# Kernel tuning notes

Hardware: AMD Instinct MI355X
Metric: run time of the kernel (lower is better)

Reference implementation:

```python
import jax, jax.numpy as jnp
import numpy as np

V, E, H = 50000, 200, 256
B, R, S, W = 16, 16, 16, 32


def gru_last(x, Wih, Whh, bih, bhh):
    """PyTorch-style GRU, return final hidden state.
    x: [N, T, D]; Wih: [3H, D]; Whh: [3H, H]. Gate order: r, z, n."""
    gx = jnp.einsum('ntd,gd->ntg', x, Wih) + bih  # precompute input gates [N,T,3H]
    h0 = jnp.zeros((x.shape[0], Whh.shape[1]), x.dtype)

    def step(h, gxt):
        gh = h @ Whh.T + bhh
        xr, xz, xn = jnp.split(gxt, 3, axis=-1)
        hr, hz, hn = jnp.split(gh, 3, axis=-1)
        r = jax.nn.sigmoid(xr + hr)
        z = jax.nn.sigmoid(xz + hz)
        n = jnp.tanh(xn + r * hn)
        return (1.0 - z) * n + z * h, None

    h, _ = jax.lax.scan(step, h0, jnp.swapaxes(gx, 0, 1))
    return h  # [N, H]


def mlp(x, W1, b1, W2, b2):
    # Linear -> SELU -> (Dropout is identity in eval) -> Linear
    return jax.nn.selu(x @ W1.T + b1) @ W2.T + b2


def setup_inputs() -> dict:
    key = jax.random.key(0)
    ks = jax.random.split(key, 20)
    n = lambda k, shp: (jax.random.normal(k, shp, dtype=jnp.float32) * 0.05)
    inp = {
        'inputs': jax.random.randint(ks[0], (B, R, S, W), 0, V, dtype=jnp.int64),
        'emb': n(ks[1], (V, E)),
        'w_Wih': n(ks[2], (3 * H, E)), 'w_Whh': n(ks[3], (3 * H, H)),
        'w_bih': n(ks[4], (3 * H,)), 'w_bhh': n(ks[5], (3 * H,)),
        's_Wih': n(ks[6], (3 * H, H)), 's_Whh': n(ks[7], (3 * H, H)),
        's_bih': n(ks[8], (3 * H,)), 's_bhh': n(ks[9], (3 * H,)),
        'r_Wih': n(ks[10], (3 * H, H)), 'r_Whh': n(ks[11], (3 * H, H)),
        'r_bih': n(ks[12], (3 * H,)), 'r_bhh': n(ks[13], (3 * H,)),
        'rfc_W1': n(ks[14], (H // 2, H)), 'rfc_b1': n(ks[15], (H // 2,)),
        'rfc_W2': n(ks[16], (1, H // 2)), 'rfc_b2': jnp.zeros((1,), jnp.float32),
        'pfc_W1': n(ks[17], (H // 2, H)), 'pfc_b1': n(ks[18], (H // 2,)),
        'pfc_W2': n(ks[19], (1, H // 2)), 'pfc_b2': jnp.zeros((1,), jnp.float32),
    }
    return inp


def reference(inputs, emb, w_Wih, w_Whh, w_bih, w_bhh,
              s_Wih, s_Whh, s_bih, s_bhh,
              r_Wih, r_Whh, r_bih, r_bhh,
              rfc_W1, rfc_b1, rfc_W2, rfc_b2,
              pfc_W1, pfc_b1, pfc_W2, pfc_b2):
    b, r, s, w = inputs.shape
    x = emb[inputs]                                   # [B,R,S,W,E] (dropout = identity in eval)
    # word-level GRU over all sentences at once (batches the Python double loop)
    sent_h = gru_last(x.reshape(b * r * s, w, E), w_Wih, w_Whh, w_bih, w_bhh)  # [B*R*S, H]
    # sentence-level GRU per review
    rev_h = gru_last(sent_h.reshape(b * r, s, H), s_Wih, s_Whh, s_bih, s_bhh)  # [B*R, H]
    p_batch = rev_h.reshape(b, r, H)                  # [B, R, H]
    r_stars = mlp(p_batch, rfc_W1, rfc_b1, rfc_W2, rfc_b2)  # [B, R, 1]
    # review-level GRU per business
    biz_h = gru_last(p_batch, r_Wih, r_Whh, r_bih, r_bhh)   # [B, H]
    b_stars = mlp(biz_h, pfc_W1, pfc_b1, pfc_W2, pfc_b2)    # [B, 1]
    return (b_stars, r_stars)
```

## Files before the change

### kernel.cpp

```cpp
#include <hip/hip_runtime.h>
#include <math.h>

#define VOCAB 50000
#define EDIM  200
#define HDIM  256
#define G3    768
#define NSEQ1 4096
#define T1    32
#define NSEQ2 256
#define T2    16
#define NSEQ3 16
#define T3    16

using bf16x8 = __attribute__((ext_vector_type(8))) short;
using f32x4  = __attribute__((ext_vector_type(4))) float;

__device__ __forceinline__ float sigmoid_f(float x) {
    return 1.0f / (1.0f + __expf(-x));
}
__device__ __forceinline__ float tanh_f(float x) {
    return 1.0f - 2.0f / (__expf(2.0f * x) + 1.0f);
}
__device__ __forceinline__ short f2b(float f) {
    unsigned u = __float_as_uint(f);
    unsigned r = (u + 0x7fffu + ((u >> 16) & 1u)) >> 16;
    return (short)r;
}
__device__ __forceinline__ float b2f(unsigned short v) {
    return __uint_as_float((unsigned)v << 16);
}
__device__ __forceinline__ void lds_barrier() {
    asm volatile("s_waitcnt lgkmcnt(0)\n\ts_barrier" ::: "memory");
}

struct CvtJob { const float* src; short* dst; int kin; int kpad; };
struct CvtJobs { CvtJob j[6]; };

__global__ void convert6(CvtJobs jobs) {
    const CvtJob jb = jobs.j[blockIdx.y];
    const int r = blockIdx.x;
    for (int k = threadIdx.x; k < jb.kpad; k += blockDim.x)
        jb.dst[(size_t)r * jb.kpad + k] =
            (k < jb.kin) ? f2b(jb.src[(size_t)r * jb.kin + k]) : (short)0;
}

template <int KC, bool AF32, bool CBF16>
__global__ __launch_bounds__(512) void gemm_mfma(
    const void* __restrict__ Av, const short* __restrict__ WB,
    const float* __restrict__ bias, void* __restrict__ Cv,
    int M, int Keff) {
    constexpr int KPAD  = KC * 32;
    constexpr int CELLS = KPAD / 8;
    __shared__ short As[128 * 256];
    const int tid = threadIdx.x;
    const int m0 = blockIdx.x * 128;
    const int n0 = blockIdx.y * 192;

    {
        const int row  = tid >> 2;
        const int c0   = (tid & 3) * 8;
        const int rowg = m0 + row;
        const int vcell = Keff >> 3;
        for (int i = 0; i < 8; i++) {
            const int c = c0 + i;
            if (c >= CELLS) break;
            bf16x8 v;
            if (rowg < M && c < vcell) {
                if constexpr (AF32) {
                    const float* ap = (const float*)Av + (size_t)rowg * Keff + c * 8;
                    const float4 x = *(const float4*)ap;
                    const float4 y = *(const float4*)(ap + 4);
                    v[0] = f2b(x.x); v[1] = f2b(x.y); v[2] = f2b(x.z); v[3] = f2b(x.w);
                    v[4] = f2b(y.x); v[5] = f2b(y.y); v[6] = f2b(y.z); v[7] = f2b(y.w);
                } else {
                    const short* ap = (const short*)Av + (size_t)rowg * Keff + c * 8;
                    v = *(const bf16x8*)ap;
                }
            } else {
                v = (bf16x8)(short)0;
            }
            *(bf16x8*)&As[row * 256 + ((c ^ (row & 7)) << 3)] = v;
        }
    }
    __syncthreads();

    const int w  = tid >> 6;
    const int l  = tid & 63;
    const int lr = l & 15, lg = l >> 4;

    bf16x8 af[KC];
    {
        const int row = (w << 4) + lr;
#pragma unroll
        for (int kc = 0; kc < KC; kc++) {
            const int cell = kc * 4 + lg;
            af[kc] = *(const bf16x8*)&As[row * 256 + ((cell ^ (row & 7)) << 3)];
        }
    }
    f32x4 acc[12];
#pragma unroll
    for (int nt = 0; nt < 12; nt++) acc[nt] = (f32x4){0.f, 0.f, 0.f, 0.f};
#pragma unroll
    for (int nt = 0; nt < 12; nt++) {
        const short* wb = WB + (size_t)(n0 + nt * 16 + lr) * KPAD + lg * 8;
#pragma unroll
        for (int kc = 0; kc < KC; kc++) {
            bf16x8 bf = *(const bf16x8*)(wb + kc * 32);
            acc[nt] = __builtin_amdgcn_mfma_f32_16x16x32_bf16(af[kc], bf, acc[nt], 0, 0, 0);
        }
    }
#pragma unroll
    for (int nt = 0; nt < 12; nt++) {
        const int col = n0 + nt * 16 + lr;
        const float bv = bias[col];
#pragma unroll
        for (int q = 0; q < 4; q++) {
            const int row = m0 + (w << 4) + lg * 4 + q;
            if (row < M) {
                const float o = acc[nt][q] + bv;
                if constexpr (CBF16) ((short*)Cv)[(size_t)row * G3 + col] = f2b(o);
                else                 ((float*)Cv)[(size_t)row * G3 + col] = o;
            }
        }
    }
}

__global__ __launch_bounds__(512, 2) void gru_mfma(
    const int* __restrict__ idx,
    const short* __restrict__ gxb,
    const short* __restrict__ WB,
    const float* __restrict__ bhh,
    float* __restrict__ hf32,
    short* __restrict__ hb16,
    int T) {
    __shared__ short wsN[256 * 256 / 2 * 2];
    __shared__ short hsB[16 * 256];
    __shared__ int idxs[16 * T1];
    const int tid = threadIdx.x;
    const int n0 = blockIdx.x * 16;
    const int w  = tid >> 6, l = tid & 63;
    const int lr = l & 15, lg = l >> 4;
    const int tt0 = w * 2;
    const int jj0 = tt0 * 16 + lr;
    const int jj1 = jj0 + 16;

    for (int i = tid; i < 16 * 256; i += 512) hsB[i] = 0;
    if (idx) {
        for (int i = tid; i < 16 * T; i += 512) {
            const int s = i / T, p = i - s * T;
            int tk = idx[(size_t)(n0 + s) * T + p];
            idxs[s * T + p] = min(max(tk, 0), VOCAB - 1);
        }
    }
#pragma unroll
    for (int i = 0; i < 16; i++) {
        const int cellidx = tid * 16 + i;
        const int rr = cellidx >> 5;
        const int cc = cellidx & 31;
        bf16x8 v = *(const bf16x8*)&WB[(size_t)(512 + rr) * 256 + cc * 8];
        *(bf16x8*)&wsN[rr * 256 + ((cc ^ (rr & 7)) << 3)] = v;
    }

    bf16x8 bwR[2][8], bwZ[2][8];
#pragma unroll
    for (int ti = 0; ti < 2; ti++) {
        const int jjt = (tt0 + ti) * 16 + lr;
#pragma unroll
        for (int kc = 0; kc < 8; kc++) {
            bwR[ti][kc] = *(const bf16x8*)&WB[(size_t)jjt * 256 + kc * 32 + lg * 8];
            bwZ[ti][kc] = *(const bf16x8*)&WB[(size_t)(256 + jjt) * 256 + kc * 32 + lg * 8];
        }
    }
    const float bR0 = bhh[jj0],       bR1 = bhh[jj1];
    const float bZ0 = bhh[256 + jj0], bZ1 = bhh[256 + jj1];
    const float bN0 = bhh[512 + jj0], bN1 = bhh[512 + jj1];

    float hreg[2][4] = {};
    __syncthreads();

    unsigned gA[12], gB[12];
    auto load_gx = [&](unsigned (&buf)[12], int t) {
#pragma unroll
        for (int q = 0; q < 4; q++) {
            const int s = lg * 4 + q;
            size_t rowbase;
            if (idx) rowbase = (size_t)idxs[s * T + t] * G3;
            else     rowbase = ((size_t)(n0 + s) * T + t) * G3;
            const unsigned short* src = (const unsigned short*)(gxb + rowbase);
            const unsigned xr0 = src[jj0],       xr1 = src[jj1];
            const unsigned xz0 = src[256 + jj0], xz1 = src[256 + jj1];
            const unsigned xn0 = src[512 + jj0], xn1 = src[512 + jj1];
            buf[q * 3 + 0] = xr0 | (xz0 << 16);
            buf[q * 3 + 1] = xr1 | (xz1 << 16);
            buf[q * 3 + 2] = xn0 | (xn1 << 16);
        }
    };

    auto step = [&](const unsigned (&buf)[12]) {
        f32x4 aR[2], aZ[2], aN[2];
#pragma unroll
        for (int ti = 0; ti < 2; ti++) {
            aR[ti] = (f32x4){0.f, 0.f, 0.f, 0.f};
            aZ[ti] = (f32x4){0.f, 0.f, 0.f, 0.f};
            aN[ti] = (f32x4){0.f, 0.f, 0.f, 0.f};
        }
#pragma unroll
        for (int kc = 0; kc < 8; kc++) {
            const int cell = kc * 4 + lg;
            const bf16x8 a  = *(const bf16x8*)&hsB[lr * 256 + ((cell ^ (lr & 7)) << 3)];
            const bf16x8 n0f = *(const bf16x8*)&wsN[jj0 * 256 + ((cell ^ (jj0 & 7)) << 3)];
            const bf16x8 n1f = *(const bf16x8*)&wsN[jj1 * 256 + ((cell ^ (jj1 & 7)) << 3)];
            aR[0] = __builtin_amdgcn_mfma_f32_16x16x32_bf16(a, bwR[0][kc], aR[0], 0, 0, 0);
            aZ[0] = __builtin_amdgcn_mfma_f32_16x16x32_bf16(a, bwZ[0][kc], aZ[0], 0, 0, 0);
            aN[0] = __builtin_amdgcn_mfma_f32_16x16x32_bf16(a, n0f, aN[0], 0, 0, 0);
            aR[1] = __builtin_amdgcn_mfma_f32_16x16x32_bf16(a, bwR[1][kc], aR[1], 0, 0, 0);
            aZ[1] = __builtin_amdgcn_mfma_f32_16x16x32_bf16(a, bwZ[1][kc], aZ[1], 0, 0, 0);
            aN[1] = __builtin_amdgcn_mfma_f32_16x16x32_bf16(a, n1f, aN[1], 0, 0, 0);
        }
        lds_barrier();

#pragma unroll
        for (int q = 0; q < 4; q++) {
            const int s = lg * 4 + q;
            const unsigned prz0 = buf[q * 3 + 0];
            const unsigned prz1 = buf[q * 3 + 1];
            const unsigned pn   = buf[q * 3 + 2];
            {
                const float xr = b2f((unsigned short)(prz0 & 0xffff));
                const float xz = b2f((unsigned short)(prz0 >> 16));
                const float xn = b2f((unsigned short)(pn & 0xffff));
                const float r = sigmoid_f(xr + aR[0][q] + bR0);
                const float z = sigmoid_f(xz + aZ[0][q] + bZ0);
                const float n = tanh_f(xn + r * (aN[0][q] + bN0));
                const float h = (1.f - z) * n + z * hreg[0][q];
                hreg[0][q] = h;
                hsB[s * 256 + (((jj0 >> 3) ^ (s & 7)) << 3) + (jj0 & 7)] = f2b(h);
            }
            {
                const float xr = b2f((unsigned short)(prz1 & 0xffff));
                const float xz = b2f((unsigned short)(prz1 >> 16));
                const float xn = b2f((unsigned short)(pn >> 16));
                const float r = sigmoid_f(xr + aR[1][q] + bR1);
                const float z = sigmoid_f(xz + aZ[1][q] + bZ1);
                const float n = tanh_f(xn + r * (aN[1][q] + bN1));
                const float h = (1.f - z) * n + z * hreg[1][q];
                hreg[1][q] = h;
                hsB[s * 256 + (((jj1 >> 3) ^ (s & 7)) << 3) + (jj1 & 7)] = f2b(h);
            }
        }
        lds_barrier();
    };

    load_gx(gA, 0);
    for (int t = 0; t < T; t += 2) {
        if (t + 1 < T) load_gx(gB, t + 1);
        step(gA);
        if (t + 2 < T) load_gx(gA, t + 2);
        step(gB);
    }

#pragma unroll
    for (int q = 0; q < 4; q++) {
        const int s = lg * 4 + q;
        const size_t o0 = (size_t)(n0 + s) * HDIM + jj0;
        const size_t o1 = (size_t)(n0 + s) * HDIM + jj1;
        if (hf32) { hf32[o0] = hreg[0][q]; hf32[o1] = hreg[1][q]; }
        if (hb16) { hb16[o0] = f2b(hreg[0][q]); hb16[o1] = f2b(hreg[1][q]); }
    }
}

__global__ __launch_bounds__(128) void mlp_head(
    const float* __restrict__ hin, const float* __restrict__ W1,
    const float* __restrict__ b1, const float* __restrict__ W2,
    const float* __restrict__ b2, float* __restrict__ out) {
    const int row = blockIdx.x;
    const int gg = threadIdx.x;
    const float* h = hin + (size_t)row * HDIM;
    const float* wv1 = W1 + (size_t)gg * HDIM;
    float acc = 0.f;
#pragma unroll 4
    for (int k = 0; k < HDIM; k += 4) {
        const float4 hv = *(const float4*)&h[k];
        const float4 wv = *(const float4*)&wv1[k];
        acc += hv.x * wv.x; acc += hv.y * wv.y;
        acc += hv.z * wv.z; acc += hv.w * wv.w;
    }
    acc += b1[gg];
    const float alpha = 1.6732632423543772f;
    const float scale = 1.0507009873554805f;
    const float s = scale * (acc > 0.f ? acc : alpha * expm1f(acc));
    float v = s * W2[gg];

    __shared__ float red[128];
    red[gg] = v;
    __syncthreads();
    if (gg < 64) {
        float x = red[gg] + red[gg + 64];
#pragma unroll
        for (int off = 32; off; off >>= 1) x += __shfl_down(x, off);
        if (gg == 0) out[row] = x + b2[0];
    }
}

extern "C" void kernel_launch(void* const* d_in, const int* in_sizes, int n_in,
                              void* d_out, int out_size, void* d_ws, size_t ws_size,
                              hipStream_t stream) {
    const int*   idx    = (const int*)d_in[0];
    const float* emb    = (const float*)d_in[1];
    const float* w_Wih  = (const float*)d_in[2];
    const float* w_Whh  = (const float*)d_in[3];
    const float* w_bih  = (const float*)d_in[4];
    const float* w_bhh  = (const float*)d_in[5];
    const float* s_Wih  = (const float*)d_in[6];
    const float* s_Whh  = (const float*)d_in[7];
    const float* s_bih  = (const float*)d_in[8];
    const float* s_bhh  = (const float*)d_in[9];
    const float* r_Wih  = (const float*)d_in[10];
    const float* r_Whh  = (const float*)d_in[11];
    const float* r_bih  = (const float*)d_in[12];
    const float* r_bhh  = (const float*)d_in[13];
    const float* rfc_W1 = (const float*)d_in[14];
    const float* rfc_b1 = (const float*)d_in[15];
    const float* rfc_W2 = (const float*)d_in[16];
    const float* rfc_b2 = (const float*)d_in[17];
    const float* pfc_W1 = (const float*)d_in[18];
    const float* pfc_b1 = (const float*)d_in[19];
    const float* pfc_W2 = (const float*)d_in[20];
    const float* pfc_b2 = (const float*)d_in[21];

    float* out = (float*)d_out;

    short* sws = (short*)d_ws;
    short* Pb      = sws;
    short* gx2b    = Pb      + (size_t)VOCAB * G3;
    short* gx3b    = gx2b    + (size_t)NSEQ1 * G3;
    short* WhhB_w  = gx3b    + (size_t)NSEQ2 * G3;
    short* WihB_w  = WhhB_w  + (size_t)G3 * HDIM;
    short* sWihB   = WihB_w  + (size_t)G3 * 224;
    short* sWhhB   = sWihB   + (size_t)G3 * HDIM;
    short* rWihB   = sWhhB   + (size_t)G3 * HDIM;
    short* rWhhB   = rWihB   + (size_t)G3 * HDIM;
    short* sent_hB = rWhhB   + (size_t)G3 * HDIM;
    short* rev_hB  = sent_hB + (size_t)NSEQ1 * HDIM;
    float* fws     = (float*)(rev_hB + (size_t)NSEQ2 * HDIM);
    float* rev_h   = fws;
    float* biz_h   = rev_h + (size_t)NSEQ2 * HDIM;

    CvtJobs jobs;
    jobs.j[0] = {w_Whh, WhhB_w, HDIM, HDIM};
    jobs.j[1] = {w_Wih, WihB_w, EDIM, 224};
    jobs.j[2] = {s_Wih, sWihB, HDIM, HDIM};
    jobs.j[3] = {s_Whh, sWhhB, HDIM, HDIM};
    jobs.j[4] = {r_Wih, rWihB, HDIM, HDIM};
    jobs.j[5] = {r_Whh, rWhhB, HDIM, HDIM};
    convert6<<<dim3(G3, 6), 256, 0, stream>>>(jobs);

    gemm_mfma<7, true, true><<<dim3((VOCAB + 127) / 128, 4), 512, 0, stream>>>(
        emb, WihB_w, w_bih, Pb, VOCAB, EDIM);

    gru_mfma<<<NSEQ1 / 16, 512, 0, stream>>>(
        idx, Pb, WhhB_w, w_bhh, nullptr, sent_hB, T1);

    gemm_mfma<8, false, true><<<dim3(NSEQ1 / 128, 4), 512, 0, stream>>>(
        sent_hB, sWihB, s_bih, gx2b, NSEQ1, HDIM);

    gru_mfma<<<NSEQ2 / 16, 512, 0, stream>>>(
        nullptr, gx2b, sWhhB, s_bhh, rev_h, rev_hB, T2);

    mlp_head<<<NSEQ2, 128, 0, stream>>>(
        rev_h, rfc_W1, rfc_b1, rfc_W2, rfc_b2, out + 16);

    gemm_mfma<8, false, true><<<dim3(2, 4), 512, 0, stream>>>(
        rev_hB, rWihB, r_bih, gx3b, NSEQ2, HDIM);

    gru_mfma<<<1, 512, 0, stream>>>(
        nullptr, gx3b, rWhhB, r_bhh, biz_h, nullptr, T3);

    mlp_head<<<NSEQ3, 128, 0, stream>>>(
        biz_h, pfc_W1, pfc_b1, pfc_W2, pfc_b2, out);
}
```

Before: 626.8 us.

## Interleave gate-projection output layout, double-buffer GRU hidden state, fuse MLP heads

The GEMM epilogue now writes the r/z/n gate pre-activations in a permuted, packed layout, so each GRU lane fetches its six bf16 gate inputs with one 12-byte load instead of six scattered 2-byte loads. The GRU hidden state in shared memory is double-buffered, which removes one of the two barriers per timestep. The separate MLP head kernels are folded into the tail of the sentence- and review-level GRU kernels, dropping two launches and the fp32 hidden-state round trip through global memory. In exchange, LDS use per block grows by 8 KB, and the single-block final GRU now also runs a serial 128-term reduction per output.

```diff
diff --git a/kernel.cpp b/kernel.cpp
--- a/kernel.cpp
+++ b/kernel.cpp
@@ -44,10 +44,10 @@
             (k < jb.kin) ? f2b(jb.src[(size_t)r * jb.kin + k]) : (short)0;
 }
 
-template <int KC, bool AF32, bool CBF16>
+template <int KC, bool AF32>
 __global__ __launch_bounds__(512) void gemm_mfma(
     const void* __restrict__ Av, const short* __restrict__ WB,
-    const float* __restrict__ bias, void* __restrict__ Cv,
+    const float* __restrict__ bias, unsigned* __restrict__ Cv,
     int M, int Keff) {
     constexpr int KPAD  = KC * 32;
     constexpr int CELLS = KPAD / 8;
@@ -109,17 +109,22 @@
             acc[nt] = __builtin_amdgcn_mfma_f32_16x16x32_bf16(af[kc], bf, acc[nt], 0, 0, 0);
         }
     }
-#pragma unroll
-    for (int nt = 0; nt < 12; nt++) {
-        const int col = n0 + nt * 16 + lr;
-        const float bv = bias[col];
+    const int by12 = blockIdx.y * 12;
+#pragma unroll
+    for (int nt = 0; nt < 12; nt += 2) {
+        const int gt = by12 + nt;
+        const int g  = gt >> 4;
+        const int pp = (gt & 15) >> 1;
+        const int uoff = pp * 48 + lr * 3 + g;
+        const float bv0 = bias[n0 + nt * 16 + lr];
+        const float bv1 = bias[n0 + (nt + 1) * 16 + lr];
 #pragma unroll
         for (int q = 0; q < 4; q++) {
             const int row = m0 + (w << 4) + lg * 4 + q;
             if (row < M) {
-                const float o = acc[nt][q] + bv;
-                if constexpr (CBF16) ((short*)Cv)[(size_t)row * G3 + col] = f2b(o);
-                else                 ((float*)Cv)[(size_t)row * G3 + col] = o;
+                const unsigned lo = (unsigned short)f2b(acc[nt][q] + bv0);
+                const unsigned hi = (unsigned short)f2b(acc[nt + 1][q] + bv1);
+                Cv[(size_t)row * 384 + uoff] = lo | (hi << 16);
             }
         }
     }
@@ -130,21 +135,25 @@
     const short* __restrict__ gxb,
     const short* __restrict__ WB,
     const float* __restrict__ bhh,
-    float* __restrict__ hf32,
     short* __restrict__ hb16,
+    const float* __restrict__ mW1,
+    const float* __restrict__ mb1,
+    const float* __restrict__ mW2,
+    const float* __restrict__ mb2,
+    float* __restrict__ mOut,
     int T) {
-    __shared__ short wsN[256 * 256 / 2 * 2];
-    __shared__ short hsB[16 * 256];
+    __shared__ __align__(16) short wsN[256 * 256];
+    __shared__ __align__(16) short hs0[16 * 256];
+    __shared__ __align__(16) short hs1[16 * 256];
     __shared__ int idxs[16 * T1];
     const int tid = threadIdx.x;
     const int n0 = blockIdx.x * 16;
     const int w  = tid >> 6, l = tid & 63;
     const int lr = l & 15, lg = l >> 4;
-    const int tt0 = w * 2;
-    const int jj0 = tt0 * 16 + lr;
+    const int jj0 = w * 32 + lr;
     const int jj1 = jj0 + 16;
 
-    for (int i = tid; i < 16 * 256; i += 512) hsB[i] = 0;
+    for (int i = tid; i < 16 * 256; i += 512) hs0[i] = 0;
     if (idx) {
         for (int i = tid; i < 16 * T; i += 512) {
             const int s = i / T, p = i - s * T;
@@ -160,11 +169,10 @@
         bf16x8 v = *(const bf16x8*)&WB[(size_t)(512 + rr) * 256 + cc * 8];
         *(bf16x8*)&wsN[rr * 256 + ((cc ^ (rr & 7)) << 3)] = v;
     }
-
     bf16x8 bwR[2][8], bwZ[2][8];
 #pragma unroll
     for (int ti = 0; ti < 2; ti++) {
-        const int jjt = (tt0 + ti) * 16 + lr;
+        const int jjt = (w * 2 + ti) * 16 + lr;
 #pragma unroll
         for (int kc = 0; kc < 8; kc++) {
             bwR[ti][kc] = *(const bf16x8*)&WB[(size_t)jjt * 256 + kc * 32 + lg * 8];
@@ -178,25 +186,19 @@
     float hreg[2][4] = {};
     __syncthreads();
 
-    unsigned gA[12], gB[12];
-    auto load_gx = [&](unsigned (&buf)[12], int t) {
+    uint3 gA[4], gB[4];
+    auto load_gx = [&](uint3 (&buf)[4], int t) {
 #pragma unroll
         for (int q = 0; q < 4; q++) {
             const int s = lg * 4 + q;
             size_t rowbase;
             if (idx) rowbase = (size_t)idxs[s * T + t] * G3;
             else     rowbase = ((size_t)(n0 + s) * T + t) * G3;
-            const unsigned short* src = (const unsigned short*)(gxb + rowbase);
-            const unsigned xr0 = src[jj0],       xr1 = src[jj1];
-            const unsigned xz0 = src[256 + jj0], xz1 = src[256 + jj1];
-            const unsigned xn0 = src[512 + jj0], xn1 = src[512 + jj1];
-            buf[q * 3 + 0] = xr0 | (xz0 << 16);
-            buf[q * 3 + 1] = xr1 | (xz1 << 16);
-            buf[q * 3 + 2] = xn0 | (xn1 << 16);
+            buf[q] = *(const uint3*)(gxb + rowbase + w * 96 + lr * 6);
         }
     };
 
-    auto step = [&](const unsigned (&buf)[12]) {
+    auto step = [&](const uint3 (&buf)[4], const short* hsR, short* hsW) {
         f32x4 aR[2], aZ[2], aN[2];
 #pragma unroll
         for (int ti = 0; ti < 2; ti++) {
@@ -207,7 +209,7 @@
 #pragma unroll
         for (int kc = 0; kc < 8; kc++) {
             const int cell = kc * 4 + lg;
-            const bf16x8 a  = *(const bf16x8*)&hsB[lr * 256 + ((cell ^ (lr & 7)) << 3)];
+            const bf16x8 a   = *(const bf16x8*)&hsR[lr * 256 + ((cell ^ (lr & 7)) << 3)];
             const bf16x8 n0f = *(const bf16x8*)&wsN[jj0 * 256 + ((cell ^ (jj0 & 7)) << 3)];
             const bf16x8 n1f = *(const bf16x8*)&wsN[jj1 * 256 + ((cell ^ (jj1 & 7)) << 3)];
             aR[0] = __builtin_amdgcn_mfma_f32_16x16x32_bf16(a, bwR[0][kc], aR[0], 0, 0, 0);
@@ -217,35 +219,31 @@
             aZ[1] = __builtin_amdgcn_mfma_f32_16x16x32_bf16(a, bwZ[1][kc], aZ[1], 0, 0, 0);
             aN[1] = __builtin_amdgcn_mfma_f32_16x16x32_bf16(a, n1f, aN[1], 0, 0, 0);
         }
-        lds_barrier();
-
 #pragma unroll
         for (int q = 0; q < 4; q++) {
             const int s = lg * 4 + q;
-            const unsigned prz0 = buf[q * 3 + 0];
-            const unsigned prz1 = buf[q * 3 + 1];
-            const unsigned pn   = buf[q * 3 + 2];
+            const uint3 u = buf[q];
             {
-                const float xr = b2f((unsigned short)(prz0 & 0xffff));
-                const float xz = b2f((unsigned short)(prz0 >> 16));
-                const float xn = b2f((unsigned short)(pn & 0xffff));
+                const float xr = b2f((unsigned short)(u.x & 0xffff));
+                const float xz = b2f((unsigned short)(u.y & 0xffff));
+                const float xn = b2f((unsigned short)(u.z & 0xffff));
                 const float r = sigmoid_f(xr + aR[0][q] + bR0);
                 const float z = sigmoid_f(xz + aZ[0][q] + bZ0);
                 const float n = tanh_f(xn + r * (aN[0][q] + bN0));
                 const float h = (1.f - z) * n + z * hreg[0][q];
                 hreg[0][q] = h;
-                hsB[s * 256 + (((jj0 >> 3) ^ (s & 7)) << 3) + (jj0 & 7)] = f2b(h);
+                hsW[s * 256 + (((jj0 >> 3) ^ (s & 7)) << 3) + (jj0 & 7)] = f2b(h);
             }
             {
-                const float xr = b2f((unsigned short)(prz1 & 0xffff));
-                const float xz = b2f((unsigned short)(prz1 >> 16));
-                const float xn = b2f((unsigned short)(pn >> 16));
+                const float xr = b2f((unsigned short)(u.x >> 16));
+                const float xz = b2f((unsigned short)(u.y >> 16));
+                const float xn = b2f((unsigned short)(u.z >> 16));
                 const float r = sigmoid_f(xr + aR[1][q] + bR1);
                 const float z = sigmoid_f(xz + aZ[1][q] + bZ1);
                 const float n = tanh_f(xn + r * (aN[1][q] + bN1));
                 const float h = (1.f - z) * n + z * hreg[1][q];
                 hreg[1][q] = h;
-                hsB[s * 256 + (((jj1 >> 3) ^ (s & 7)) << 3) + (jj1 & 7)] = f2b(h);
+                hsW[s * 256 + (((jj1 >> 3) ^ (s & 7)) << 3) + (jj1 & 7)] = f2b(h);
             }
         }
         lds_barrier();
@@ -254,51 +252,57 @@
     load_gx(gA, 0);
     for (int t = 0; t < T; t += 2) {
         if (t + 1 < T) load_gx(gB, t + 1);
-        step(gA);
+        step(gA, hs0, hs1);
         if (t + 2 < T) load_gx(gA, t + 2);
-        step(gB);
-    }
-
-#pragma unroll
-    for (int q = 0; q < 4; q++) {
-        const int s = lg * 4 + q;
-        const size_t o0 = (size_t)(n0 + s) * HDIM + jj0;
-        const size_t o1 = (size_t)(n0 + s) * HDIM + jj1;
-        if (hf32) { hf32[o0] = hreg[0][q]; hf32[o1] = hreg[1][q]; }
-        if (hb16) { hb16[o0] = f2b(hreg[0][q]); hb16[o1] = f2b(hreg[1][q]); }
-    }
-}
-
-__global__ __launch_bounds__(128) void mlp_head(
-    const float* __restrict__ hin, const float* __restrict__ W1,
-    const float* __restrict__ b1, const float* __restrict__ W2,
-    const float* __restrict__ b2, float* __restrict__ out) {
-    const int row = blockIdx.x;
-    const int gg = threadIdx.x;
-    const float* h = hin + (size_t)row * HDIM;
-    const float* wv1 = W1 + (size_t)gg * HDIM;
-    float acc = 0.f;
+        step(gB, hs1, hs0);
+    }
+
+    if (hb16) {
+#pragma unroll
+        for (int q = 0; q < 4; q++) {
+            const int s = lg * 4 + q;
+            hb16[(size_t)(n0 + s) * HDIM + jj0] = f2b(hreg[0][q]);
+            hb16[(size_t)(n0 + s) * HDIM + jj1] = f2b(hreg[1][q]);
+        }
+    }
+    if (mW1) {
+        float* hf = (float*)wsN;
+#pragma unroll
+        for (int q = 0; q < 4; q++) {
+            const int s = lg * 4 + q;
+            hf[s * HDIM + jj0] = hreg[0][q];
+            hf[s * HDIM + jj1] = hreg[1][q];
+        }
+        lds_barrier();
+        const int mm = tid & 127;
+        const int sg = tid >> 7;
+        const float* w1 = mW1 + (size_t)mm * HDIM;
+        const float b1v = mb1[mm];
+        const float w2v = mW2[mm];
+        float* redf = (float*)hs0;
+#pragma unroll
+        for (int si = 0; si < 4; si++) {
+            const int s = si * 4 + sg;
+            const float* hrow = hf + s * HDIM;
+            float d = 0.f;
 #pragma unroll 4
-    for (int k = 0; k < HDIM; k += 4) {
-        const float4 hv = *(const float4*)&h[k];
-        const float4 wv = *(const float4*)&wv1[k];
-        acc += hv.x * wv.x; acc += hv.y * wv.y;
-        acc += hv.z * wv.z; acc += hv.w * wv.w;
-    }
-    acc += b1[gg];
-    const float alpha = 1.6732632423543772f;
-    const float scale = 1.0507009873554805f;
-    const float s = scale * (acc > 0.f ? acc : alpha * expm1f(acc));
-    float v = s * W2[gg];
-
-    __shared__ float red[128];
-    red[gg] = v;
-    __syncthreads();
-    if (gg < 64) {
-        float x = red[gg] + red[gg + 64];
-#pragma unroll
-        for (int off = 32; off; off >>= 1) x += __shfl_down(x, off);
-        if (gg == 0) out[row] = x + b2[0];
+            for (int k = 0; k < HDIM; k += 4) {
+                const float4 a = *(const float4*)&hrow[k];
+                const float4 b = *(const float4*)&w1[k];
+                d += a.x * b.x; d += a.y * b.y; d += a.z * b.z; d += a.w * b.w;
+            }
+            d += b1v;
+            const float alpha = 1.6732632423543772f;
+            const float scale = 1.0507009873554805f;
+            const float sv = scale * (d > 0.f ? d : alpha * expm1f(d));
+            redf[s * 128 + mm] = sv * w2v;
+        }
+        lds_barrier();
+        if (tid < 16) {
+            float accv = mb2[0];
+            for (int m = 0; m < 128; m++) accv += redf[tid * 128 + m];
+            mOut[n0 + tid] = accv;
+        }
     }
 }
 
@@ -342,9 +346,6 @@
     short* rWhhB   = rWihB   + (size_t)G3 * HDIM;
     short* sent_hB = rWhhB   + (size_t)G3 * HDIM;
     short* rev_hB  = sent_hB + (size_t)NSEQ1 * HDIM;
-    float* fws     = (float*)(rev_hB + (size_t)NSEQ2 * HDIM);
-    float* rev_h   = fws;
-    float* biz_h   = rev_h + (size_t)NSEQ2 * HDIM;
 
     CvtJobs jobs;
     jobs.j[0] = {w_Whh, WhhB_w, HDIM, HDIM};
@@ -355,27 +356,24 @@
     jobs.j[5] = {r_Whh, rWhhB, HDIM, HDIM};
     convert6<<<dim3(G3, 6), 256, 0, stream>>>(jobs);
 
-    gemm_mfma<7, true, true><<<dim3((VOCAB + 127) / 128, 4), 512, 0, stream>>>(
-        emb, WihB_w, w_bih, Pb, VOCAB, EDIM);
+    gemm_mfma<7, true><<<dim3((VOCAB + 127) / 128, 4), 512, 0, stream>>>(
+        emb, WihB_w, w_bih, (unsigned*)Pb, VOCAB, EDIM);
 
     gru_mfma<<<NSEQ1 / 16, 512, 0, stream>>>(
-        idx, Pb, WhhB_w, w_bhh, nullptr, sent_hB, T1);
-
-    gemm_mfma<8, false, true><<<dim3(NSEQ1 / 128, 4), 512, 0, stream>>>(
-        sent_hB, sWihB, s_bih, gx2b, NSEQ1, HDIM);
+        idx, Pb, WhhB_w, w_bhh, sent_hB,
+        nullptr, nullptr, nullptr, nullptr, nullptr, T1);
+
+    gemm_mfma<8, false><<<dim3(NSEQ1 / 128, 4), 512, 0, stream>>>(
+        sent_hB, sWihB, s_bih, (unsigned*)gx2b, NSEQ1, HDIM);
 
     gru_mfma<<<NSEQ2 / 16, 512, 0, stream>>>(
-        nullptr, gx2b, sWhhB, s_bhh, rev_h, rev_hB, T2);
-
-    mlp_head<<<NSEQ2, 128, 0, stream>>>(
-        rev_h, rfc_W1, rfc_b1, rfc_W2, rfc_b2, out + 16);
-
-    gemm_mfma<8, false, true><<<dim3(2, 4), 512, 0, stream>>>(
-        rev_hB, rWihB, r_bih, gx3b, NSEQ2, HDIM);
+        nullptr, gx2b, sWhhB, s_bhh, rev_hB,
+        rfc_W1, rfc_b1, rfc_W2, rfc_b2, out + 16, T2);
+
+    gemm_mfma<8, false><<<dim3(2, 4), 512, 0, stream>>>(
+        rev_hB, rWihB, r_bih, (unsigned*)gx3b, NSEQ2, HDIM);
 
     gru_mfma<<<1, 512, 0, stream>>>(
-        nullptr, gx3b, rWhhB, r_bhh, biz_h, nullptr, T3);
-
-    mlp_head<<<NSEQ3, 128, 0, stream>>>(
-        biz_h, pfc_W1, pfc_b1, pfc_W2, pfc_b2, out);
-}
+        nullptr, gx3b, rWhhB, r_bhh, nullptr,
+        pfc_W1, pfc_b1, pfc_W2, pfc_b2, out, T3);
+}
```

Measured after the change: 728.5 us. 1.16x slower.
